# Kernel tuning notes

Measured on AMD Instinct MI355X. Metric: run time of the kernel, lower is better.

## Reference

```python
import jax, jax.numpy as jnp
import numpy as np

N_NODES = 100000
N_EDGES = 3200000
IN_FEATS = 128
OUT_FEATS = 64


def setup_inputs() -> dict:
    key = jax.random.key(0)
    k1, k2, k3, k4 = jax.random.split(key, 4)
    in_feat = jax.random.normal(k1, (N_NODES, IN_FEATS), dtype=jnp.float32)
    src = jax.random.randint(k2, (N_EDGES,), 0, N_NODES, dtype=jnp.int64)
    dst = jax.random.randint(k3, (N_EDGES,), 0, N_NODES, dtype=jnp.int64)
    W = jax.random.normal(k4, (IN_FEATS, OUT_FEATS), dtype=jnp.float32) / np.sqrt(IN_FEATS)
    b = jnp.zeros((OUT_FEATS,), dtype=jnp.float32)
    return {"in_feat": in_feat, "src": src, "dst": dst, "W": W, "b": b}


def reference(in_feat, src, dst, W, b):
    n = in_feat.shape[0]
    ones = jnp.ones_like(src, dtype=in_feat.dtype)
    # DGL GraphConv norm='both': scale by out-degree(src)^-1/2 before agg,
    # in-degree(dst)^-1/2 after agg. Clamp degree to >=1 for isolated nodes.
    deg_out = jnp.maximum(jax.ops.segment_sum(ones, src, num_segments=n), 1.0)
    deg_in = jnp.maximum(jax.ops.segment_sum(ones, dst, num_segments=n), 1.0)
    # in_feats > out_feats => apply W first (mult-first path in DGL)
    xw = in_feat @ W  # [N, out]
    msg = xw[src] * jax.lax.rsqrt(deg_out)[src][:, None]  # [E, out]
    agg = jax.ops.segment_sum(msg, dst, num_segments=n)  # [N, out]
    h = agg * jax.lax.rsqrt(deg_in)[:, None] + b
    return jax.nn.relu(h)
```

## Files before the change

### kernel.cpp

```cpp
#include <hip/hip_runtime.h>
#include <hip/hip_bf16.h>


constexpr int N_NODES = 100000;
constexpr int N_EDGES = 3200000;
constexpr int IN_F    = 128;
constexpr int OUT_F   = 64;
constexpr int BUCKET_NODES = 256;
constexpr int NB   = (N_NODES + BUCKET_NODES - 1) / BUCKET_NODES;
constexpr int CAPB = 10240;
constexpr int C_CHUNK  = 4096;
constexpr int C_BLOCKS = (N_EDGES + C_CHUNK - 1) / C_CHUNK;
constexpr int G_TILE   = 32;
constexpr int G_BLOCKS = 1024;
constexpr int G_GROUPS = N_NODES / G_TILE;

__global__ __launch_bounds__(512) void partition_kernel(
        const int* __restrict__ src, const int* __restrict__ dst,
        int* __restrict__ bucket_cnt, int* __restrict__ bucket_cnt2,
        unsigned* __restrict__ pairs, unsigned char* __restrict__ sbytes) {
    __shared__ int l_cnt [NB], l_base [NB], l_pos [NB], g_base [NB];
    __shared__ int l_cnt2[NB], l_base2[NB], l_pos2[NB], g_base2[NB];
    __shared__ int wsum_s[8];
    __shared__ unsigned buf[C_CHUNK];
    __shared__ unsigned short bkt_of[C_CHUNK];
    __shared__ unsigned char  bbuf[C_CHUNK];
    __shared__ unsigned short bkt2_of[C_CHUNK];
    const int tid  = threadIdx.x;
    const int lane = tid & 63;
    const int wid  = tid >> 6;
    const long e0 = (long)blockIdx.x * C_CHUNK;
    const int  cn = (int)min((long)C_CHUNK, (long)N_EDGES - e0);
    const int  cn4 = cn >> 2;

    for (int i = tid; i < NB; i += 512) { l_cnt[i] = 0; l_cnt2[i] = 0; }
    __syncthreads();

    unsigned r_pk[8];
    short    r_bk[8];
    const int4* d4p = (const int4*)(dst + e0);
    const int4* s4p = (const int4*)(src + e0);
    #pragma unroll
    for (int k = 0; k < 2; ++k) {
        int i4 = tid + k * 512;
        int rb = k * 4;
        if (i4 < cn4) {
            int4 d4 = d4p[i4];
            int4 s4 = s4p[i4];
            int dd[4] = {d4.x, d4.y, d4.z, d4.w};
            int ss[4] = {s4.x, s4.y, s4.z, s4.w};
            #pragma unroll
            for (int j = 0; j < 4; ++j) {
                int bk = dd[j] >> 8;
                r_bk[rb + j] = (short)bk;
                r_pk[rb + j] = ((unsigned)(dd[j] & 255) << 17) | (unsigned)ss[j];
                atomicAdd(&l_cnt[bk], 1);
                atomicAdd(&l_cnt2[ss[j] >> 8], 1);
            }
        } else {
            #pragma unroll
            for (int j = 0; j < 4; ++j) r_bk[rb + j] = -1;
        }
    }
    __syncthreads();

    {
        int v = (tid < NB) ? l_cnt[tid] : 0;
        int inc = v;
        #pragma unroll
        for (int off = 1; off < 64; off <<= 1) {
            int t = __shfl_up(inc, off);
            if (lane >= off) inc += t;
        }
        if (lane == 63) wsum_s[wid] = inc;
        __syncthreads();
        int woff = 0;
        #pragma unroll
        for (int w = 0; w < 8; ++w) if (w < wid) woff += wsum_s[w];
        int excl = woff + inc - v;
        if (tid < NB) {
            l_base[tid] = excl;
            l_pos[tid]  = excl;
            g_base[tid] = v ? atomicAdd(&bucket_cnt[tid], v) : 0;
        }
    }
    __syncthreads();
    {
        int v = (tid < NB) ? l_cnt2[tid] : 0;
        int inc = v;
        #pragma unroll
        for (int off = 1; off < 64; off <<= 1) {
            int t = __shfl_up(inc, off);
            if (lane >= off) inc += t;
        }
        if (lane == 63) wsum_s[wid] = inc;
        __syncthreads();
        int woff = 0;
        #pragma unroll
        for (int w = 0; w < 8; ++w) if (w < wid) woff += wsum_s[w];
        int excl = woff + inc - v;
        if (tid < NB) {
            l_base2[tid] = excl;
            l_pos2[tid]  = excl;
            g_base2[tid] = v ? atomicAdd(&bucket_cnt2[tid], v) : 0;
        }
    }
    __syncthreads();

    #pragma unroll
    for (int k = 0; k < 8; ++k) {
        if (r_bk[k] >= 0) {
            unsigned pk = r_pk[k];
            int p = atomicAdd(&l_pos[(int)r_bk[k]], 1);
            buf[p] = pk;
            bkt_of[p] = (unsigned short)r_bk[k];
            int bk2 = (int)((pk >> 8) & 0x1FF);
            int p2 = atomicAdd(&l_pos2[bk2], 1);
            bbuf[p2] = (unsigned char)(pk & 255);
            bkt2_of[p2] = (unsigned short)bk2;
        }
    }
    __syncthreads();

    for (int i = tid; i < cn; i += 512) {
        int bk = bkt_of[i];
        int gp = g_base[bk] + (i - l_base[bk]);
        if (gp < CAPB)
            pairs[(long)bk * CAPB + gp] = buf[i];
        int b2 = bkt2_of[i];
        int gp2 = g_base2[b2] + (i - l_base2[b2]);
        if (gp2 < CAPB)
            sbytes[(long)b2 * CAPB + gp2] = bbuf[i];
    }
}

__global__ __launch_bounds__(256) void count_kernel(
        const unsigned char* __restrict__ sbytes, const int* __restrict__ bucket_cnt2,
        int* __restrict__ deg_out_i) {
    __shared__ int hist[BUCKET_NODES];
    const int tid = threadIdx.x;
    const int bk  = blockIdx.x;
    hist[tid] = 0;
    __syncthreads();

    const int cnt = min(bucket_cnt2[bk], CAPB);
    const unsigned* sb4 = (const unsigned*)(sbytes + (long)bk * CAPB);
    const int n4 = cnt >> 2;
    for (int i = tid; i < n4; i += 256) {
        unsigned u = sb4[i];
        atomicAdd(&hist[u & 255], 1);
        atomicAdd(&hist[(u >> 8) & 255], 1);
        atomicAdd(&hist[(u >> 16) & 255], 1);
        atomicAdd(&hist[u >> 24], 1);
    }
    for (int i = (n4 << 2) + tid; i < cnt; i += 256)
        atomicAdd(&hist[sbytes[(long)bk * CAPB + i]], 1);
    __syncthreads();

    const int node = bk * BUCKET_NODES + tid;
    if (node < N_NODES) deg_out_i[node] = hist[tid];
}

__global__ __launch_bounds__(512) void mega_kernel(
        unsigned* __restrict__ pairs, const int* __restrict__ bucket_cnt,
        int* __restrict__ row_beg, int* __restrict__ row_deg,
        const float* __restrict__ x, const float* __restrict__ W,
        const int* __restrict__ deg_out_i, __hip_bfloat16* __restrict__ sxw) {
    alignas(16) __shared__ char smem[49152];
    const int tid = threadIdx.x;

    if (blockIdx.x < NB) {
        unsigned* buf  = (unsigned*)smem;
        int*      hist = (int*)(smem + 40960);
        int*      cur  = (int*)(smem + 40960 + 1024);
        int*      wsum = (int*)(smem + 40960 + 2048);
        const int lane = tid & 63;
        const int wid  = tid >> 6;
        const int bk   = blockIdx.x;
        const long base = (long)bk * CAPB;
        const int cnt  = min(bucket_cnt[bk], CAPB);

        if (tid < 256) hist[tid] = 0;
        __syncthreads();

        const int c4 = cnt >> 2;
        const uint4* p4 = (const uint4*)(pairs + base);
        for (int i4 = tid; i4 < c4; i4 += 512) {
            uint4 e4 = p4[i4];
            ((uint4*)buf)[i4] = e4;
            atomicAdd(&hist[e4.x >> 17], 1);
            atomicAdd(&hist[e4.y >> 17], 1);
            atomicAdd(&hist[e4.z >> 17], 1);
            atomicAdd(&hist[e4.w >> 17], 1);
        }
        for (int i = (c4 << 2) + tid; i < cnt; i += 512) {
            unsigned e = pairs[base + i];
            buf[i] = e;
            atomicAdd(&hist[e >> 17], 1);
        }
        __syncthreads();

        int v = (tid < 256) ? hist[tid] : 0;
        int inc = v;
        #pragma unroll
        for (int off = 1; off < 64; off <<= 1) {
            int t = __shfl_up(inc, off);
            if (lane >= off) inc += t;
        }
        if (tid < 256 && lane == 63) wsum[wid] = inc;
        __syncthreads();
        if (tid < 256) {
            int woff = 0;
            #pragma unroll
            for (int w = 0; w < 4; ++w) if (w < wid) woff += wsum[w];
            int excl = woff + inc - v;
            cur[tid] = excl;
            const int node = bk * BUCKET_NODES + tid;
            if (node < N_NODES) {
                row_beg[node] = (int)(base + excl);
                row_deg[node] = v;
            }
        }
        __syncthreads();

        for (int i = tid; i < cnt; i += 512) {
            unsigned e = buf[i];
            int p = atomicAdd(&cur[e >> 17], 1);
            pairs[base + p] = e & 0x1FFFF;
        }
    } else {
        float* Wl = (float*)smem;
        float* xl = (float*)(smem + 32768);
        for (int i = tid; i < IN_F * OUT_F; i += 512) Wl[i] = W[i];

        const int sub = tid >> 6;
        const int col = tid & 63;
        const int bid = blockIdx.x - NB;

        for (int g = bid; g < G_GROUPS; g += G_BLOCKS) {
            __syncthreads();
            const float4* xg = (const float4*)(x + (long)g * G_TILE * IN_F);
            float4* xl4 = (float4*)xl;
            xl4[tid]       = xg[tid];
            xl4[tid + 512] = xg[tid + 512];
            __syncthreads();

            float a0 = 0.0f, a1 = 0.0f, a2 = 0.0f, a3 = 0.0f;
            const float* xr = xl + sub * 4 * IN_F;
            #pragma unroll
            for (int k4 = 0; k4 < IN_F / 4; ++k4) {
                float4 x0 = ((const float4*)xr)[k4];
                float4 x1 = ((const float4*)(xr + IN_F))[k4];
                float4 x2 = ((const float4*)(xr + 2 * IN_F))[k4];
                float4 x3 = ((const float4*)(xr + 3 * IN_F))[k4];
                float w0 = Wl[(k4 * 4 + 0) * OUT_F + col];
                float w1 = Wl[(k4 * 4 + 1) * OUT_F + col];
                float w2 = Wl[(k4 * 4 + 2) * OUT_F + col];
                float w3 = Wl[(k4 * 4 + 3) * OUT_F + col];
                a0 += x0.x * w0 + x0.y * w1 + x0.z * w2 + x0.w * w3;
                a1 += x1.x * w0 + x1.y * w1 + x1.z * w2 + x1.w * w3;
                a2 += x2.x * w0 + x2.y * w1 + x2.z * w2 + x2.w * w3;
                a3 += x3.x * w0 + x3.y * w1 + x3.z * w2 + x3.w * w3;
            }

            const int r0 = g * G_TILE + sub * 4;
            int d0 = deg_out_i[r0 + 0], d1 = deg_out_i[r0 + 1];
            int d2 = deg_out_i[r0 + 2], d3 = deg_out_i[r0 + 3];
            float s0 = rsqrtf((float)(d0 < 1 ? 1 : d0));
            float s1 = rsqrtf((float)(d1 < 1 ? 1 : d1));
            float s2 = rsqrtf((float)(d2 < 1 ? 1 : d2));
            float s3 = rsqrtf((float)(d3 < 1 ? 1 : d3));
            sxw[(long)(r0 + 0) * OUT_F + col] = __float2bfloat16(a0 * s0);
            sxw[(long)(r0 + 1) * OUT_F + col] = __float2bfloat16(a1 * s1);
            sxw[(long)(r0 + 2) * OUT_F + col] = __float2bfloat16(a2 * s2);
            sxw[(long)(r0 + 3) * OUT_F + col] = __float2bfloat16(a3 * s3);
        }
    }
}

#define ACC8(u)                                   \
    a0 += __uint_as_float((u).x << 16);           \
    a1 += __uint_as_float((u).x & 0xFFFF0000u);   \
    a2 += __uint_as_float((u).y << 16);           \
    a3 += __uint_as_float((u).y & 0xFFFF0000u);   \
    a4 += __uint_as_float((u).z << 16);           \
    a5 += __uint_as_float((u).z & 0xFFFF0000u);   \
    a6 += __uint_as_float((u).w << 16);           \
    a7 += __uint_as_float((u).w & 0xFFFF0000u);

__global__ __launch_bounds__(256) void gather_kernel(
        const int* __restrict__ row_beg, const int* __restrict__ row_deg,
        const unsigned* __restrict__ csr_src, const uint4* __restrict__ sxw4,
        const float* __restrict__ b, float* __restrict__ out) {
    const int lane = threadIdx.x & 63;
    const int node = blockIdx.x * 4 + (threadIdx.x >> 6);

    const int eo = lane >> 3;
    const int c  = lane & 7;

    const int beg = row_beg[node];
    const int deg = row_deg[node];
    const int end = beg + deg;

    float a0 = 0, a1 = 0, a2 = 0, a3 = 0, a4 = 0, a5 = 0, a6 = 0, a7 = 0;

    int j = beg;
    for (; j + 32 <= end; j += 32) {
        unsigned s0 = csr_src[j + eo];
        unsigned s1 = csr_src[j + 8 + eo];
        unsigned s2 = csr_src[j + 16 + eo];
        unsigned s3 = csr_src[j + 24 + eo];
        uint4 u0 = sxw4[(long)s0 * 8 + c];
        uint4 u1 = sxw4[(long)s1 * 8 + c];
        uint4 u2 = sxw4[(long)s2 * 8 + c];
        uint4 u3 = sxw4[(long)s3 * 8 + c];
        ACC8(u0) ACC8(u1) ACC8(u2) ACC8(u3)
    }
    for (; j + 8 <= end; j += 8) {
        unsigned s = csr_src[j + eo];
        uint4 u = sxw4[(long)s * 8 + c];
        ACC8(u)
    }
    if (j < end) {
        int e = j + eo;
        if (e < end) {
            unsigned s = csr_src[e];
            uint4 u = sxw4[(long)s * 8 + c];
            ACC8(u)
        }
    }

    #pragma unroll
    for (int off = 8; off < 64; off <<= 1) {
        a0 += __shfl_xor(a0, off);
        a1 += __shfl_xor(a1, off);
        a2 += __shfl_xor(a2, off);
        a3 += __shfl_xor(a3, off);
        a4 += __shfl_xor(a4, off);
        a5 += __shfl_xor(a5, off);
        a6 += __shfl_xor(a6, off);
        a7 += __shfl_xor(a7, off);
    }

    if (lane < 8) {
        float d = (float)(deg < 1 ? 1 : deg);
        float s = rsqrtf(d);
        float4 b0 = ((const float4*)b)[c * 2];
        float4 b1 = ((const float4*)b)[c * 2 + 1];
        float4 o0, o1;
        o0.x = a0 * s + b0.x; o0.x = o0.x > 0.0f ? o0.x : 0.0f;
        o0.y = a1 * s + b0.y; o0.y = o0.y > 0.0f ? o0.y : 0.0f;
        o0.z = a2 * s + b0.z; o0.z = o0.z > 0.0f ? o0.z : 0.0f;
        o0.w = a3 * s + b0.w; o0.w = o0.w > 0.0f ? o0.w : 0.0f;
        o1.x = a4 * s + b1.x; o1.x = o1.x > 0.0f ? o1.x : 0.0f;
        o1.y = a5 * s + b1.y; o1.y = o1.y > 0.0f ? o1.y : 0.0f;
        o1.z = a6 * s + b1.z; o1.z = o1.z > 0.0f ? o1.z : 0.0f;
        o1.w = a7 * s + b1.w; o1.w = o1.w > 0.0f ? o1.w : 0.0f;
        float4* orow = (float4*)(out + (long)node * OUT_F);
        orow[c * 2]     = o0;
        orow[c * 2 + 1] = o1;
    }
}

extern "C" void kernel_launch(void* const* d_in, const int* in_sizes, int n_in,
                              void* d_out, int out_size, void* d_ws, size_t ws_size,
                              hipStream_t stream) {
    const float* in_feat = (const float*)d_in[0];
    const int*   src     = (const int*)d_in[1];
    const int*   dst     = (const int*)d_in[2];
    const float* W       = (const float*)d_in[3];
    const float* b       = (const float*)d_in[4];
    float*       out     = (float*)d_out;

    __hip_bfloat16* sxw         = (__hip_bfloat16*)d_ws;
    int*            deg_out_i   = (int*)(sxw + (size_t)N_NODES * OUT_F);
    int*            bucket_cnt  = deg_out_i + N_NODES;
    int*            bucket_cnt2 = bucket_cnt + NB;
    int*            row_beg     = bucket_cnt2 + NB;
    int*            row_deg     = row_beg + N_NODES;
    unsigned*       pairs       = (unsigned*)(row_deg + N_NODES);
    unsigned char*  sbytes      = (unsigned char*)(pairs + (size_t)NB * CAPB);

    hipMemsetAsync(bucket_cnt, 0, 2 * (size_t)NB * sizeof(int), stream);

    partition_kernel<<<C_BLOCKS, 512, 0, stream>>>(src, dst, bucket_cnt,
                                                   bucket_cnt2, pairs, sbytes);

    count_kernel<<<NB, 256, 0, stream>>>(sbytes, bucket_cnt2, deg_out_i);

    mega_kernel<<<NB + G_BLOCKS, 512, 0, stream>>>(pairs, bucket_cnt,
                                                   row_beg, row_deg,
                                                   in_feat, W, deg_out_i, sxw);

    gather_kernel<<<N_NODES / 4, 256, 0, stream>>>(row_beg, row_deg, pairs,
                                                   (const uint4*)sxw, b, out);
}
```

Before: 260.0 us.

## Count out-degree with replicated global atomics and retile the XW GEMM

Out-degree counting moves off the second bucket partition (byte scatter plus a histogram kernel) and onto direct global atomics into four replicated degree arrays. A small kernel then sums the replicas and precomputes the rsqrt scale. The XW projection is retiled so each thread computes four output columns of one row using float4 W loads and a padded x tile, and writes packed bf16 through a custom round-to-nearest-even conversion. This cuts partition shared-memory traffic and one scatter pass, at the cost of about 3.2M global atomics spread over a small number of replicas.

```diff
diff --git a/kernel.cpp b/kernel.cpp
--- a/kernel.cpp
+++ b/kernel.cpp
@@ -14,26 +14,32 @@
 constexpr int G_TILE   = 32;
 constexpr int G_BLOCKS = 1024;
 constexpr int G_GROUPS = N_NODES / G_TILE;
+constexpr int XLS      = 136;
+constexpr int NREP     = 4;
+
+static __device__ __forceinline__ unsigned short f2bf(float f) {
+    unsigned u = __float_as_uint(f);
+    u += 0x7fffu + ((u >> 16) & 1u);
+    return (unsigned short)(u >> 16);
+}
 
 __global__ __launch_bounds__(512) void partition_kernel(
         const int* __restrict__ src, const int* __restrict__ dst,
-        int* __restrict__ bucket_cnt, int* __restrict__ bucket_cnt2,
-        unsigned* __restrict__ pairs, unsigned char* __restrict__ sbytes) {
-    __shared__ int l_cnt [NB], l_base [NB], l_pos [NB], g_base [NB];
-    __shared__ int l_cnt2[NB], l_base2[NB], l_pos2[NB], g_base2[NB];
+        int* __restrict__ bucket_cnt, unsigned* __restrict__ pairs,
+        int* __restrict__ deg4) {
+    __shared__ int l_cnt[NB], l_base[NB], l_pos[NB], g_base[NB];
     __shared__ int wsum_s[8];
     __shared__ unsigned buf[C_CHUNK];
     __shared__ unsigned short bkt_of[C_CHUNK];
-    __shared__ unsigned char  bbuf[C_CHUNK];
-    __shared__ unsigned short bkt2_of[C_CHUNK];
     const int tid  = threadIdx.x;
     const int lane = tid & 63;
     const int wid  = tid >> 6;
     const long e0 = (long)blockIdx.x * C_CHUNK;
     const int  cn = (int)min((long)C_CHUNK, (long)N_EDGES - e0);
     const int  cn4 = cn >> 2;
-
-    for (int i = tid; i < NB; i += 512) { l_cnt[i] = 0; l_cnt2[i] = 0; }
+    int* mydeg = deg4 + (size_t)(blockIdx.x & (NREP - 1)) * N_NODES;
+
+    for (int i = tid; i < NB; i += 512) l_cnt[i] = 0;
     __syncthreads();
 
     unsigned r_pk[8];
@@ -55,7 +61,7 @@
                 r_bk[rb + j] = (short)bk;
                 r_pk[rb + j] = ((unsigned)(dd[j] & 255) << 17) | (unsigned)ss[j];
                 atomicAdd(&l_cnt[bk], 1);
-                atomicAdd(&l_cnt2[ss[j] >> 8], 1);
+                atomicAdd(&mydeg[ss[j]], 1);
             }
         } else {
             #pragma unroll
@@ -85,39 +91,13 @@
         }
     }
     __syncthreads();
-    {
-        int v = (tid < NB) ? l_cnt2[tid] : 0;
-        int inc = v;
-        #pragma unroll
-        for (int off = 1; off < 64; off <<= 1) {
-            int t = __shfl_up(inc, off);
-            if (lane >= off) inc += t;
-        }
-        if (lane == 63) wsum_s[wid] = inc;
-        __syncthreads();
-        int woff = 0;
-        #pragma unroll
-        for (int w = 0; w < 8; ++w) if (w < wid) woff += wsum_s[w];
-        int excl = woff + inc - v;
-        if (tid < NB) {
-            l_base2[tid] = excl;
-            l_pos2[tid]  = excl;
-            g_base2[tid] = v ? atomicAdd(&bucket_cnt2[tid], v) : 0;
-        }
-    }
-    __syncthreads();
 
     #pragma unroll
     for (int k = 0; k < 8; ++k) {
         if (r_bk[k] >= 0) {
-            unsigned pk = r_pk[k];
             int p = atomicAdd(&l_pos[(int)r_bk[k]], 1);
-            buf[p] = pk;
+            buf[p] = r_pk[k];
             bkt_of[p] = (unsigned short)r_bk[k];
-            int bk2 = (int)((pk >> 8) & 0x1FF);
-            int p2 = atomicAdd(&l_pos2[bk2], 1);
-            bbuf[p2] = (unsigned char)(pk & 255);
-            bkt2_of[p2] = (unsigned short)bk2;
         }
     }
     __syncthreads();
@@ -127,46 +107,26 @@
         int gp = g_base[bk] + (i - l_base[bk]);
         if (gp < CAPB)
             pairs[(long)bk * CAPB + gp] = buf[i];
-        int b2 = bkt2_of[i];
-        int gp2 = g_base2[b2] + (i - l_base2[b2]);
-        if (gp2 < CAPB)
-            sbytes[(long)b2 * CAPB + gp2] = bbuf[i];
-    }
-}
-
-__global__ __launch_bounds__(256) void count_kernel(
-        const unsigned char* __restrict__ sbytes, const int* __restrict__ bucket_cnt2,
-        int* __restrict__ deg_out_i) {
-    __shared__ int hist[BUCKET_NODES];
-    const int tid = threadIdx.x;
-    const int bk  = blockIdx.x;
-    hist[tid] = 0;
-    __syncthreads();
-
-    const int cnt = min(bucket_cnt2[bk], CAPB);
-    const unsigned* sb4 = (const unsigned*)(sbytes + (long)bk * CAPB);
-    const int n4 = cnt >> 2;
-    for (int i = tid; i < n4; i += 256) {
-        unsigned u = sb4[i];
-        atomicAdd(&hist[u & 255], 1);
-        atomicAdd(&hist[(u >> 8) & 255], 1);
-        atomicAdd(&hist[(u >> 16) & 255], 1);
-        atomicAdd(&hist[u >> 24], 1);
-    }
-    for (int i = (n4 << 2) + tid; i < cnt; i += 256)
-        atomicAdd(&hist[sbytes[(long)bk * CAPB + i]], 1);
-    __syncthreads();
-
-    const int node = bk * BUCKET_NODES + tid;
-    if (node < N_NODES) deg_out_i[node] = hist[tid];
+    }
+}
+
+__global__ __launch_bounds__(256) void rsq_kernel(
+        const int* __restrict__ deg4, float* __restrict__ rsq_out) {
+    const int node = blockIdx.x * 256 + threadIdx.x;
+    if (node < N_NODES) {
+        int d = 0;
+        #pragma unroll
+        for (int r = 0; r < NREP; ++r) d += deg4[(size_t)r * N_NODES + node];
+        rsq_out[node] = rsqrtf((float)(d < 1 ? 1 : d));
+    }
 }
 
 __global__ __launch_bounds__(512) void mega_kernel(
         unsigned* __restrict__ pairs, const int* __restrict__ bucket_cnt,
         int* __restrict__ row_beg, int* __restrict__ row_deg,
         const float* __restrict__ x, const float* __restrict__ W,
-        const int* __restrict__ deg_out_i, __hip_bfloat16* __restrict__ sxw) {
-    alignas(16) __shared__ char smem[49152];
+        const float* __restrict__ rsq_out, __hip_bfloat16* __restrict__ sxw) {
+    alignas(16) __shared__ char smem[50176];
     const int tid = threadIdx.x;
 
     if (blockIdx.x < NB) {
@@ -233,47 +193,42 @@
         float* xl = (float*)(smem + 32768);
         for (int i = tid; i < IN_F * OUT_F; i += 512) Wl[i] = W[i];
 
-        const int sub = tid >> 6;
-        const int col = tid & 63;
+        const int r  = tid >> 4;
+        const int c4 = tid & 15;
+        const float4* Wl4 = (const float4*)Wl;
         const int bid = blockIdx.x - NB;
 
         for (int g = bid; g < G_GROUPS; g += G_BLOCKS) {
             __syncthreads();
             const float4* xg = (const float4*)(x + (long)g * G_TILE * IN_F);
-            float4* xl4 = (float4*)xl;
-            xl4[tid]       = xg[tid];
-            xl4[tid + 512] = xg[tid + 512];
+            #pragma unroll
+            for (int k = 0; k < 2; ++k) {
+                int i = tid + k * 512;
+                int row = i >> 5, q = i & 31;
+                ((float4*)xl)[row * (XLS / 4) + q] = xg[i];
+            }
             __syncthreads();
 
-            float a0 = 0.0f, a1 = 0.0f, a2 = 0.0f, a3 = 0.0f;
-            const float* xr = xl + sub * 4 * IN_F;
+            float4 a = {0.0f, 0.0f, 0.0f, 0.0f};
+            const float4* xr4 = (const float4*)(xl + r * XLS);
             #pragma unroll
             for (int k4 = 0; k4 < IN_F / 4; ++k4) {
-                float4 x0 = ((const float4*)xr)[k4];
-                float4 x1 = ((const float4*)(xr + IN_F))[k4];
-                float4 x2 = ((const float4*)(xr + 2 * IN_F))[k4];
-                float4 x3 = ((const float4*)(xr + 3 * IN_F))[k4];
-                float w0 = Wl[(k4 * 4 + 0) * OUT_F + col];
-                float w1 = Wl[(k4 * 4 + 1) * OUT_F + col];
-                float w2 = Wl[(k4 * 4 + 2) * OUT_F + col];
-                float w3 = Wl[(k4 * 4 + 3) * OUT_F + col];
-                a0 += x0.x * w0 + x0.y * w1 + x0.z * w2 + x0.w * w3;
-                a1 += x1.x * w0 + x1.y * w1 + x1.z * w2 + x1.w * w3;
-                a2 += x2.x * w0 + x2.y * w1 + x2.z * w2 + x2.w * w3;
-                a3 += x3.x * w0 + x3.y * w1 + x3.z * w2 + x3.w * w3;
+                float4 xv = xr4[k4];
+                float4 w0 = Wl4[(k4 * 4 + 0) * 16 + c4];
+                float4 w1 = Wl4[(k4 * 4 + 1) * 16 + c4];
+                float4 w2 = Wl4[(k4 * 4 + 2) * 16 + c4];
+                float4 w3 = Wl4[(k4 * 4 + 3) * 16 + c4];
+                a.x += xv.x * w0.x + xv.y * w1.x + xv.z * w2.x + xv.w * w3.x;
+                a.y += xv.x * w0.y + xv.y * w1.y + xv.z * w2.y + xv.w * w3.y;
+                a.z += xv.x * w0.z + xv.y * w1.z + xv.z * w2.z + xv.w * w3.z;
+                a.w += xv.x * w0.w + xv.y * w1.w + xv.z * w2.w + xv.w * w3.w;
             }
-
-            const int r0 = g * G_TILE + sub * 4;
-            int d0 = deg_out_i[r0 + 0], d1 = deg_out_i[r0 + 1];
-            int d2 = deg_out_i[r0 + 2], d3 = deg_out_i[r0 + 3];
-            float s0 = rsqrtf((float)(d0 < 1 ? 1 : d0));
-            float s1 = rsqrtf((float)(d1 < 1 ? 1 : d1));
-            float s2 = rsqrtf((float)(d2 < 1 ? 1 : d2));
-            float s3 = rsqrtf((float)(d3 < 1 ? 1 : d3));
-            sxw[(long)(r0 + 0) * OUT_F + col] = __float2bfloat16(a0 * s0);
-            sxw[(long)(r0 + 1) * OUT_F + col] = __float2bfloat16(a1 * s1);
-            sxw[(long)(r0 + 2) * OUT_F + col] = __float2bfloat16(a2 * s2);
-            sxw[(long)(r0 + 3) * OUT_F + col] = __float2bfloat16(a3 * s3);
+            const int rg = g * G_TILE + r;
+            float rs = rsq_out[rg];
+            ushort4 o;
+            o.x = f2bf(a.x * rs); o.y = f2bf(a.y * rs);
+            o.z = f2bf(a.z * rs); o.w = f2bf(a.w * rs);
+            ((ushort4*)sxw)[(long)rg * 16 + c4] = o;
         }
     }
 }
@@ -372,25 +327,24 @@
     const float* b       = (const float*)d_in[4];
     float*       out     = (float*)d_out;
 
-    __hip_bfloat16* sxw         = (__hip_bfloat16*)d_ws;
-    int*            deg_out_i   = (int*)(sxw + (size_t)N_NODES * OUT_F);
-    int*            bucket_cnt  = deg_out_i + N_NODES;
-    int*            bucket_cnt2 = bucket_cnt + NB;
-    int*            row_beg     = bucket_cnt2 + NB;
-    int*            row_deg     = row_beg + N_NODES;
-    unsigned*       pairs       = (unsigned*)(row_deg + N_NODES);
-    unsigned char*  sbytes      = (unsigned char*)(pairs + (size_t)NB * CAPB);
-
-    hipMemsetAsync(bucket_cnt, 0, 2 * (size_t)NB * sizeof(int), stream);
+    __hip_bfloat16* sxw        = (__hip_bfloat16*)d_ws;
+    int*            deg4       = (int*)(sxw + (size_t)N_NODES * OUT_F);
+    int*            bucket_cnt = deg4 + (size_t)NREP * N_NODES;
+    float*          rsq_out    = (float*)(bucket_cnt + 400);
+    int*            row_beg    = (int*)(rsq_out + N_NODES);
+    int*            row_deg    = row_beg + N_NODES;
+    unsigned*       pairs      = (unsigned*)(row_deg + N_NODES);
+
+    hipMemsetAsync(deg4, 0, ((size_t)NREP * N_NODES + 400) * sizeof(int), stream);
 
     partition_kernel<<<C_BLOCKS, 512, 0, stream>>>(src, dst, bucket_cnt,
-                                                   bucket_cnt2, pairs, sbytes);
-
-    count_kernel<<<NB, 256, 0, stream>>>(sbytes, bucket_cnt2, deg_out_i);
+                                                   pairs, deg4);
+
+    rsq_kernel<<<(N_NODES + 255) / 256, 256, 0, stream>>>(deg4, rsq_out);
 
     mega_kernel<<<NB + G_BLOCKS, 512, 0, stream>>>(pairs, bucket_cnt,
                                                    row_beg, row_deg,
-                                                   in_feat, W, deg_out_i, sxw);
+                                                   in_feat, W, rsq_out, sxw);
 
     gather_kernel<<<N_NODES / 4, 256, 0, stream>>>(row_beg, row_deg, pairs,
                                                    (const uint4*)sxw, b, out);
```

Measured after the change: 370.6 us. 42.5% more time.

## Fold degree counting into mega kernel and apply out-degree scale during gather

Applied to the files above, without the earlier changes.

Removes the separate count kernel and runs its per-bucket out-degree histogram as extra blocks of the mega kernel, writing rsqrt of the clamped degree directly. Because the GEMM no longer waits on degrees, the source-side normalization moves into the gather loop as an extra per-edge scalar load and an FMA. The GEMM is also remapped so each thread computes four output columns of one row using float4 weight reads, with padded x rows in LDS and a manual bf16 rounding. This drops one launch and one kernel dependency, at the cost of an extra random 4-byte read per edge in the gather.

```diff
diff --git a/kernel.cpp b/kernel.cpp
--- a/kernel.cpp
+++ b/kernel.cpp
@@ -14,6 +14,13 @@
 constexpr int G_TILE   = 32;
 constexpr int G_BLOCKS = 1024;
 constexpr int G_GROUPS = N_NODES / G_TILE;
+constexpr int XLS      = 136;
+
+static __device__ __forceinline__ unsigned short f2bf(float f) {
+    unsigned u = __float_as_uint(f);
+    u += 0x7fffu + ((u >> 16) & 1u);
+    return (unsigned short)(u >> 16);
+}
 
 __global__ __launch_bounds__(512) void partition_kernel(
         const int* __restrict__ src, const int* __restrict__ dst,
@@ -134,39 +141,14 @@
     }
 }
 
-__global__ __launch_bounds__(256) void count_kernel(
-        const unsigned char* __restrict__ sbytes, const int* __restrict__ bucket_cnt2,
-        int* __restrict__ deg_out_i) {
-    __shared__ int hist[BUCKET_NODES];
-    const int tid = threadIdx.x;
-    const int bk  = blockIdx.x;
-    hist[tid] = 0;
-    __syncthreads();
-
-    const int cnt = min(bucket_cnt2[bk], CAPB);
-    const unsigned* sb4 = (const unsigned*)(sbytes + (long)bk * CAPB);
-    const int n4 = cnt >> 2;
-    for (int i = tid; i < n4; i += 256) {
-        unsigned u = sb4[i];
-        atomicAdd(&hist[u & 255], 1);
-        atomicAdd(&hist[(u >> 8) & 255], 1);
-        atomicAdd(&hist[(u >> 16) & 255], 1);
-        atomicAdd(&hist[u >> 24], 1);
-    }
-    for (int i = (n4 << 2) + tid; i < cnt; i += 256)
-        atomicAdd(&hist[sbytes[(long)bk * CAPB + i]], 1);
-    __syncthreads();
-
-    const int node = bk * BUCKET_NODES + tid;
-    if (node < N_NODES) deg_out_i[node] = hist[tid];
-}
-
 __global__ __launch_bounds__(512) void mega_kernel(
         unsigned* __restrict__ pairs, const int* __restrict__ bucket_cnt,
+        const unsigned char* __restrict__ sbytes, const int* __restrict__ bucket_cnt2,
         int* __restrict__ row_beg, int* __restrict__ row_deg,
+        float* __restrict__ rsq_out,
         const float* __restrict__ x, const float* __restrict__ W,
-        const int* __restrict__ deg_out_i, __hip_bfloat16* __restrict__ sxw) {
-    alignas(16) __shared__ char smem[49152];
+        __hip_bfloat16* __restrict__ sxw) {
+    alignas(16) __shared__ char smem[50176];
     const int tid = threadIdx.x;
 
     if (blockIdx.x < NB) {
@@ -228,69 +210,91 @@
             int p = atomicAdd(&cur[e >> 17], 1);
             pairs[base + p] = e & 0x1FFFF;
         }
+    } else if (blockIdx.x < 2 * NB) {
+        int* hist = (int*)smem;
+        const int bk = blockIdx.x - NB;
+        if (tid < 256) hist[tid] = 0;
+        __syncthreads();
+
+        const int cnt = min(bucket_cnt2[bk], CAPB);
+        const unsigned* sb4 = (const unsigned*)(sbytes + (long)bk * CAPB);
+        const int n4 = cnt >> 2;
+        for (int i = tid; i < n4; i += 512) {
+            unsigned u = sb4[i];
+            atomicAdd(&hist[u & 255], 1);
+            atomicAdd(&hist[(u >> 8) & 255], 1);
+            atomicAdd(&hist[(u >> 16) & 255], 1);
+            atomicAdd(&hist[u >> 24], 1);
+        }
+        for (int i = (n4 << 2) + tid; i < cnt; i += 512)
+            atomicAdd(&hist[sbytes[(long)bk * CAPB + i]], 1);
+        __syncthreads();
+
+        if (tid < 256) {
+            const int node = bk * BUCKET_NODES + tid;
+            if (node < N_NODES) {
+                int d = hist[tid];
+                rsq_out[node] = rsqrtf((float)(d < 1 ? 1 : d));
+            }
+        }
     } else {
         float* Wl = (float*)smem;
         float* xl = (float*)(smem + 32768);
         for (int i = tid; i < IN_F * OUT_F; i += 512) Wl[i] = W[i];
 
-        const int sub = tid >> 6;
-        const int col = tid & 63;
-        const int bid = blockIdx.x - NB;
+        const int r  = tid >> 4;
+        const int c4 = tid & 15;
+        const float4* Wl4 = (const float4*)Wl;
+        const int bid = blockIdx.x - 2 * NB;
 
         for (int g = bid; g < G_GROUPS; g += G_BLOCKS) {
             __syncthreads();
             const float4* xg = (const float4*)(x + (long)g * G_TILE * IN_F);
-            float4* xl4 = (float4*)xl;
-            xl4[tid]       = xg[tid];
-            xl4[tid + 512] = xg[tid + 512];
+            #pragma unroll
+            for (int k = 0; k < 2; ++k) {
+                int i = tid + k * 512;
+                int row = i >> 5, q = i & 31;
+                ((float4*)xl)[row * (XLS / 4) + q] = xg[i];
+            }
             __syncthreads();
 
-            float a0 = 0.0f, a1 = 0.0f, a2 = 0.0f, a3 = 0.0f;
-            const float* xr = xl + sub * 4 * IN_F;
+            float4 a = {0.0f, 0.0f, 0.0f, 0.0f};
+            const float4* xr4 = (const float4*)(xl + r * XLS);
             #pragma unroll
             for (int k4 = 0; k4 < IN_F / 4; ++k4) {
-                float4 x0 = ((const float4*)xr)[k4];
-                float4 x1 = ((const float4*)(xr + IN_F))[k4];
-                float4 x2 = ((const float4*)(xr + 2 * IN_F))[k4];
-                float4 x3 = ((const float4*)(xr + 3 * IN_F))[k4];
-                float w0 = Wl[(k4 * 4 + 0) * OUT_F + col];
-                float w1 = Wl[(k4 * 4 + 1) * OUT_F + col];
-                float w2 = Wl[(k4 * 4 + 2) * OUT_F + col];
-                float w3 = Wl[(k4 * 4 + 3) * OUT_F + col];
-                a0 += x0.x * w0 + x0.y * w1 + x0.z * w2 + x0.w * w3;
-                a1 += x1.x * w0 + x1.y * w1 + x1.z * w2 + x1.w * w3;
-                a2 += x2.x * w0 + x2.y * w1 + x2.z * w2 + x2.w * w3;
-                a3 += x3.x * w0 + x3.y * w1 + x3.z * w2 + x3.w * w3;
+                float4 xv = xr4[k4];
+                float4 w0 = Wl4[(k4 * 4 + 0) * 16 + c4];
+                float4 w1 = Wl4[(k4 * 4 + 1) * 16 + c4];
+                float4 w2 = Wl4[(k4 * 4 + 2) * 16 + c4];
+                float4 w3 = Wl4[(k4 * 4 + 3) * 16 + c4];
+                a.x += xv.x * w0.x + xv.y * w1.x + xv.z * w2.x + xv.w * w3.x;
+                a.y += xv.x * w0.y + xv.y * w1.y + xv.z * w2.y + xv.w * w3.y;
+                a.z += xv.x * w0.z + xv.y * w1.z + xv.z * w2.z + xv.w * w3.z;
+                a.w += xv.x * w0.w + xv.y * w1.w + xv.z * w2.w + xv.w * w3.w;
             }
-
-            const int r0 = g * G_TILE + sub * 4;
-            int d0 = deg_out_i[r0 + 0], d1 = deg_out_i[r0 + 1];
-            int d2 = deg_out_i[r0 + 2], d3 = deg_out_i[r0 + 3];
-            float s0 = rsqrtf((float)(d0 < 1 ? 1 : d0));
-            float s1 = rsqrtf((float)(d1 < 1 ? 1 : d1));
-            float s2 = rsqrtf((float)(d2 < 1 ? 1 : d2));
-            float s3 = rsqrtf((float)(d3 < 1 ? 1 : d3));
-            sxw[(long)(r0 + 0) * OUT_F + col] = __float2bfloat16(a0 * s0);
-            sxw[(long)(r0 + 1) * OUT_F + col] = __float2bfloat16(a1 * s1);
-            sxw[(long)(r0 + 2) * OUT_F + col] = __float2bfloat16(a2 * s2);
-            sxw[(long)(r0 + 3) * OUT_F + col] = __float2bfloat16(a3 * s3);
-        }
-    }
-}
-
-#define ACC8(u)                                   \
-    a0 += __uint_as_float((u).x << 16);           \
-    a1 += __uint_as_float((u).x & 0xFFFF0000u);   \
-    a2 += __uint_as_float((u).y << 16);           \
-    a3 += __uint_as_float((u).y & 0xFFFF0000u);   \
-    a4 += __uint_as_float((u).z << 16);           \
-    a5 += __uint_as_float((u).z & 0xFFFF0000u);   \
-    a6 += __uint_as_float((u).w << 16);           \
-    a7 += __uint_as_float((u).w & 0xFFFF0000u);
+            const int rg = g * G_TILE + r;
+            ushort4 o;
+            o.x = f2bf(a.x); o.y = f2bf(a.y); o.z = f2bf(a.z); o.w = f2bf(a.w);
+            ((ushort4*)sxw)[(long)rg * 16 + c4] = o;
+        }
+    }
+}
+
+#define ACC8R(u, rs) {                                          \
+    a0 = fmaf(__uint_as_float((u).x << 16),         (rs), a0);  \
+    a1 = fmaf(__uint_as_float((u).x & 0xFFFF0000u), (rs), a1);  \
+    a2 = fmaf(__uint_as_float((u).y << 16),         (rs), a2);  \
+    a3 = fmaf(__uint_as_float((u).y & 0xFFFF0000u), (rs), a3);  \
+    a4 = fmaf(__uint_as_float((u).z << 16),         (rs), a4);  \
+    a5 = fmaf(__uint_as_float((u).z & 0xFFFF0000u), (rs), a5);  \
+    a6 = fmaf(__uint_as_float((u).w << 16),         (rs), a6);  \
+    a7 = fmaf(__uint_as_float((u).w & 0xFFFF0000u), (rs), a7);  \
+}
 
 __global__ __launch_bounds__(256) void gather_kernel(
         const int* __restrict__ row_beg, const int* __restrict__ row_deg,
         const unsigned* __restrict__ csr_src, const uint4* __restrict__ sxw4,
+        const float* __restrict__ rsq_out,
         const float* __restrict__ b, float* __restrict__ out) {
     const int lane = threadIdx.x & 63;
     const int node = blockIdx.x * 4 + (threadIdx.x >> 6);
@@ -310,23 +314,27 @@
         unsigned s1 = csr_src[j + 8 + eo];
         unsigned s2 = csr_src[j + 16 + eo];
         unsigned s3 = csr_src[j + 24 + eo];
+        float r0 = rsq_out[s0], r1 = rsq_out[s1];
+        float r2 = rsq_out[s2], r3 = rsq_out[s3];
         uint4 u0 = sxw4[(long)s0 * 8 + c];
         uint4 u1 = sxw4[(long)s1 * 8 + c];
         uint4 u2 = sxw4[(long)s2 * 8 + c];
         uint4 u3 = sxw4[(long)s3 * 8 + c];
-        ACC8(u0) ACC8(u1) ACC8(u2) ACC8(u3)
+        ACC8R(u0, r0) ACC8R(u1, r1) ACC8R(u2, r2) ACC8R(u3, r3)
     }
     for (; j + 8 <= end; j += 8) {
         unsigned s = csr_src[j + eo];
+        float rs = rsq_out[s];
         uint4 u = sxw4[(long)s * 8 + c];
-        ACC8(u)
+        ACC8R(u, rs)
     }
     if (j < end) {
         int e = j + eo;
         if (e < end) {
             unsigned s = csr_src[e];
+            float rs = rsq_out[s];
             uint4 u = sxw4[(long)s * 8 + c];
-            ACC8(u)
+            ACC8R(u, rs)
         }
     }
 
@@ -373,8 +381,8 @@
     float*       out     = (float*)d_out;
 
     __hip_bfloat16* sxw         = (__hip_bfloat16*)d_ws;
-    int*            deg_out_i   = (int*)(sxw + (size_t)N_NODES * OUT_F);
-    int*            bucket_cnt  = deg_out_i + N_NODES;
+    float*          rsq_out     = (float*)(sxw + (size_t)N_NODES * OUT_F);
+    int*            bucket_cnt  = (int*)(rsq_out + N_NODES);
     int*            bucket_cnt2 = bucket_cnt + NB;
     int*            row_beg     = bucket_cnt2 + NB;
     int*            row_deg     = row_beg + N_NODES;
@@ -386,12 +394,11 @@
     partition_kernel<<<C_BLOCKS, 512, 0, stream>>>(src, dst, bucket_cnt,
                                                    bucket_cnt2, pairs, sbytes);
 
-    count_kernel<<<NB, 256, 0, stream>>>(sbytes, bucket_cnt2, deg_out_i);
-
-    mega_kernel<<<NB + G_BLOCKS, 512, 0, stream>>>(pairs, bucket_cnt,
-                                                   row_beg, row_deg,
-                                                   in_feat, W, deg_out_i, sxw);
+    mega_kernel<<<2 * NB + G_BLOCKS, 512, 0, stream>>>(
+        pairs, bucket_cnt, sbytes, bucket_cnt2,
+        row_beg, row_deg, rsq_out, in_feat, W, sxw);
 
     gather_kernel<<<N_NODES / 4, 256, 0, stream>>>(row_beg, row_deg, pairs,
-                                                   (const uint4*)sxw, b, out);
-}
+                                                   (const uint4*)sxw, rsq_out,
+                                                   b, out);
+}
```

After: 271.6 us. 1.04x slower.
